# Kernel optimization log

Measured on AMD Instinct MI355X. Metric: run time of the kernel, lower is better.

The kernel has to match this reference:

```python
import jax, jax.numpy as jnp
import numpy as np

NUM_HEADS = 16
D_MODEL = 1024
HEAD_DIM = D_MODEL // NUM_HEADS
SCALE = float(np.sqrt(HEAD_DIM))  # NOTE: original multiplies q by sqrt(head_dim)
EPS = 1e-5


def layernorm(x, g, b):
    # LayerNorm over last dim (head_dim), learnable affine
    mu = jnp.mean(x, axis=-1, keepdims=True)
    var = jnp.mean(jnp.square(x - mu), axis=-1, keepdims=True)
    return (x - mu) * jax.lax.rsqrt(var + EPS) * g + b


def setup_inputs() -> dict:
    key = jax.random.key(0)
    ks = jax.random.split(key, 8)
    B, Nq, Nc = 2, 2048, 2048
    s = 0.02
    return {
        "x_query": jax.random.normal(ks[0], (B, Nq, D_MODEL), jnp.float32),
        "x_context": jax.random.normal(ks[1], (B, Nc, D_MODEL), jnp.float32),
        "Wq": jax.random.normal(ks[2], (D_MODEL, D_MODEL), jnp.float32) * s,
        "Wkv": jax.random.normal(ks[3], (D_MODEL, 2 * D_MODEL), jnp.float32) * s,
        "Wp": jax.random.normal(ks[4], (D_MODEL, D_MODEL), jnp.float32) * s,
        "bp": jnp.zeros((D_MODEL,), jnp.float32),
        "ln_g": jnp.ones((HEAD_DIM,), jnp.float32),
        "ln_b": jnp.zeros((HEAD_DIM,), jnp.float32),
    }


def reference(x_query, x_context, Wq, Wkv, Wp, bp, ln_g, ln_b):
    B, Nq, _ = x_query.shape
    Nc = x_context.shape[1]
    H, D = NUM_HEADS, HEAD_DIM
    # projections
    q = (x_query @ Wq).reshape(B, Nq, H, D).transpose(0, 2, 1, 3)  # b h n d
    kv = (x_context @ Wkv).reshape(B, Nc, 2, H, D)
    k = kv[:, :, 0].transpose(0, 2, 1, 3)  # b h n d
    v = kv[:, :, 1].transpose(0, 2, 1, 3)
    # QK-LayerNorm (shared params)
    q = layernorm(q, ln_g, ln_b)
    k = layernorm(k, ln_g, ln_b)
    # NOTE: faithful to source — q is MULTIPLIED by sqrt(head_dim)
    q = q * SCALE
    attn = jnp.einsum("bhqd,bhkd->bhqk", q, k)
    attn = jax.nn.softmax(attn, axis=-1)
    out = jnp.einsum("bhqk,bhkd->bhqd", attn, v)
    out = out.transpose(0, 2, 1, 3).reshape(B, Nq, H * D)
    return out @ Wp + bp
```

## Files before the change

kernel.cpp:

```cpp
#include <hip/hip_runtime.h>
#include <stdint.h>

#define NUM_HEADS 16
#define HEAD_DIM 64
#define D_MODEL 1024
#define SEQ 2048
#define BATCH 2

typedef unsigned short u16;
typedef __bf16 bf16x8 __attribute__((ext_vector_type(8)));
typedef _Float16 f16x8 __attribute__((ext_vector_type(8)));
typedef float f32x4 __attribute__((ext_vector_type(4)));

__device__ __forceinline__ u16 f2bf(float f) {
    union { float f; uint32_t u; } v; v.f = f;
    uint32_t u = v.u;
    u += 0x7FFFu + ((u >> 16) & 1u);
    return (u16)(u >> 16);
}
__device__ __forceinline__ float bf2f(u16 h) {
    union { uint32_t u; float f; } v; v.u = (uint32_t)h << 16; return v.f;
}
__device__ __forceinline__ u16 f2h(float f) {
    _Float16 h = (_Float16)f;
    return __builtin_bit_cast(u16, h);
}
__device__ __forceinline__ uint32_t pkrtz(float a, float b) {
    return __builtin_bit_cast(uint32_t, __builtin_amdgcn_cvt_pkrtz(a, b));
}

__device__ __forceinline__ bf16x8 ld8(const u16* p) {
    return *reinterpret_cast<const bf16x8*>(p);
}
__device__ __forceinline__ f16x8 ld8h(const u16* p) {
    return *reinterpret_cast<const f16x8*>(p);
}

__device__ __forceinline__ void gl_lds16(const void* g, void* l) {
    __builtin_amdgcn_global_load_lds(
        (const __attribute__((address_space(1))) void*)g,
        (__attribute__((address_space(3))) void*)l,
        16, 0, 0);
}

template <int CTRL>
__device__ __forceinline__ float dpp_mov(float x) {
    return __builtin_bit_cast(float,
        __builtin_amdgcn_update_dpp(0, __builtin_bit_cast(int, x), CTRL, 0xf, 0xf, true));
}
__device__ __forceinline__ float rowsum16(float x) {
    x += dpp_mov<0x121>(x);
    x += dpp_mov<0x122>(x);
    x += dpp_mov<0x124>(x);
    x += dpp_mov<0x128>(x);
    return x;
}

__global__ __launch_bounds__(256) void k_prep(const float* __restrict__ xq,
                                              const float* __restrict__ xc,
                                              const float* __restrict__ Wq,
                                              const float* __restrict__ Wkv,
                                              const float* __restrict__ Wp,
                                              u16* __restrict__ xq16,
                                              u16* __restrict__ xc16,
                                              u16* __restrict__ WqT16,
                                              u16* __restrict__ WkvT16,
                                              u16* __restrict__ WpT16) {
    __shared__ float tile[32][33];
    const int t = blockIdx.x;
    if (t < 8192) {
        int i = t * 256 + threadIdx.x;
        const float* src; u16* dst; int j;
        if (i < 1048576) { src = xq; dst = xq16; j = i; }
        else             { src = xc; dst = xc16; j = i - 1048576; }
        float4 v = reinterpret_cast<const float4*>(src)[j];
        ushort4 o;
        o.x = f2h(v.x); o.y = f2h(v.y); o.z = f2h(v.z); o.w = f2h(v.w);
        reinterpret_cast<ushort4*>(dst)[j] = o;
        return;
    }
    const float* W; u16* WT; int N, bi;
    if (t < 9216)       { W = Wq;  WT = WqT16;  N = 1024; bi = t - 8192; }
    else if (t < 11264) { W = Wkv; WT = WkvT16; N = 2048; bi = t - 9216; }
    else                { W = Wp;  WT = WpT16;  N = 1024; bi = t - 11264; }
    const int K = 1024;
    const int nb = N / 32;
    const int bn = (bi % nb) * 32, bk = (bi / nb) * 32;
    const int tx = threadIdx.x & 31;
    const int ty = threadIdx.x >> 5;
#pragma unroll
    for (int i = 0; i < 32; i += 8)
        tile[ty + i][tx] = W[(size_t)(bk + ty + i) * N + bn + tx];
    __syncthreads();
#pragma unroll
    for (int i = 0; i < 32; i += 8)
        WT[(size_t)(bn + ty + i) * K + bk + tx] = f2h(tile[tx][ty + i]);
}

__device__ __forceinline__ void gemm_mainloop_f16(const u16* __restrict__ A,
                                                  const u16* __restrict__ Bt,
                                                  u16* As, u16* Bs,
                                                  int tileM, int tileN, int K,
                                                  f32x4 acc[4][4]) {
    const int tid = threadIdx.x;
    const int lane = tid & 63;
    const int wv = tid >> 6;
    const int wm = wv >> 1, wn = wv & 1;
    const int quad = lane >> 4, l15 = lane & 15;

    const int c0 = tid, c1 = tid + 256;
    const u16* Ap0 = A + (size_t)(tileM + (c0 >> 2)) * K + (c0 & 3) * 8;
    const u16* Ap1 = A + (size_t)(tileM + (c1 >> 2)) * K + (c1 & 3) * 8;
    const u16* Bp0 = Bt + (size_t)(tileN + (c0 >> 2)) * K + (c0 & 3) * 8;
    const u16* Bp1 = Bt + (size_t)(tileN + (c1 >> 2)) * K + (c1 & 3) * 8;

    for (int k0 = 0; k0 < K; k0 += 32) {
        __syncthreads();
        gl_lds16(Ap0 + k0, &As[c0 * 8]);
        gl_lds16(Ap1 + k0, &As[c1 * 8]);
        gl_lds16(Bp0 + k0, &Bs[c0 * 8]);
        gl_lds16(Bp1 + k0, &Bs[c1 * 8]);
        __syncthreads();
        f16x8 af[4], bfr[4];
#pragma unroll
        for (int mi = 0; mi < 4; ++mi)
            af[mi] = ld8h(&As[(wm * 64 + mi * 16 + l15) * 32 + quad * 8]);
#pragma unroll
        for (int ni = 0; ni < 4; ++ni)
            bfr[ni] = ld8h(&Bs[(wn * 64 + ni * 16 + l15) * 32 + quad * 8]);
#pragma unroll
        for (int mi = 0; mi < 4; ++mi)
#pragma unroll
            for (int ni = 0; ni < 4; ++ni)
                acc[mi][ni] = __builtin_amdgcn_mfma_f32_16x16x32_f16(
                    af[mi], bfr[ni], acc[mi][ni], 0, 0, 0);
    }
}

#define ACC_INIT()                                                   \
    f32x4 acc[4][4];                                                 \
    _Pragma("unroll") for (int i = 0; i < 4; ++i)                    \
        _Pragma("unroll") for (int j = 0; j < 4; ++j)                \
            acc[i][j] = (f32x4){0.f, 0.f, 0.f, 0.f};

__global__ __launch_bounds__(256, 2) void k_proj_f16(const u16* __restrict__ xq16,
                                                     const u16* __restrict__ xc16,
                                                     const u16* __restrict__ WqT16,
                                                     const u16* __restrict__ WkvT16,
                                                     const float* __restrict__ lng,
                                                     const float* __restrict__ lnb,
                                                     u16* __restrict__ Qh_h,
                                                     u16* __restrict__ Qh_l,
                                                     u16* __restrict__ Kh_h,
                                                     u16* __restrict__ Kh_l,
                                                     u16* __restrict__ VT) {
    __shared__ __align__(16) u16 As[128 * 32];
    __shared__ __align__(16) u16 Bs[128 * 32];
    const int bx = blockIdx.x;
    const int tileM = blockIdx.y * 128;
    const int tid = threadIdx.x;
    const int lane = tid & 63;
    const int wv = tid >> 6;
    const int wm = wv >> 1, wn = wv & 1;
    const int quad = lane >> 4, l15 = lane & 15;
    ACC_INIT();

    if (bx < 16) {
        const bool isQ = bx < 8;
        const int tileN = (bx & 7) * 128;
        const u16* Axx = isQ ? xq16 : xc16;
        const u16* Bt  = isQ ? WqT16 : WkvT16;
        u16* Dh = isQ ? Qh_h : Kh_h;
        u16* Dl = isQ ? Qh_l : Kh_l;
        const float scl = isQ ? 8.0f : 1.0f;

        gemm_mainloop_f16(Axx, Bt, As, Bs, tileM, tileN, D_MODEL, acc);

        float gv[4], bv[4];
#pragma unroll
        for (int ni = 0; ni < 4; ++ni) { gv[ni] = lng[ni * 16 + l15]; bv[ni] = lnb[ni * 16 + l15]; }

#pragma unroll
        for (int mi = 0; mi < 4; ++mi) {
#pragma unroll
            for (int r = 0; r < 4; ++r) {
                float sum = 0.f, sq = 0.f;
#pragma unroll
                for (int ni = 0; ni < 4; ++ni) { float x = acc[mi][ni][r]; sum += x; sq += x * x; }
                sum = rowsum16(sum);
                sq  = rowsum16(sq);
                float mu = sum * (1.f / 64.f);
                float var = sq * (1.f / 64.f) - mu * mu;
                float rs = rsqrtf(var + 1e-5f);
                int m = tileM + wm * 64 + mi * 16 + quad * 4 + r;
                int bb = m >> 11, n = m & (SEQ - 1);
#pragma unroll
                for (int ni = 0; ni < 4; ++ni) {
                    int colg = tileN + wn * 64 + ni * 16 + l15;
                    int h = colg >> 6;
                    float y = ((acc[mi][ni][r] - mu) * rs * gv[ni] + bv[ni]) * scl;
                    size_t idx = (((size_t)bb * NUM_HEADS + h) * SEQ + n) * HEAD_DIM + (colg & 63);
                    u16 yh = f2bf(y);
                    Dh[idx] = yh;
                    Dl[idx] = f2bf(y - bf2f(yh));
                }
            }
        }
    } else {
        const int tileN = D_MODEL + (bx - 16) * 128;
        gemm_mainloop_f16(xc16, WkvT16, As, Bs, tileM, tileN, D_MODEL, acc);
#pragma unroll
        for (int mi = 0; mi < 4; ++mi) {
            int m0 = tileM + wm * 64 + mi * 16 + quad * 4;
            int bb = m0 >> 11, n0 = m0 & (SEQ - 1);
#pragma unroll
            for (int ni = 0; ni < 4; ++ni) {
                int colg = tileN + wn * 64 + ni * 16 + l15 - D_MODEL;
                int h = colg >> 6, d = colg & 63;
                ushort4 o;
                o.x = f2h(acc[mi][ni][0]);
                o.y = f2h(acc[mi][ni][1]);
                o.z = f2h(acc[mi][ni][2]);
                o.w = f2h(acc[mi][ni][3]);
                *reinterpret_cast<ushort4*>(
                    &VT[(((size_t)bb * NUM_HEADS + h) * HEAD_DIM + d) * SEQ + n0]) = o;
            }
        }
    }
}

__global__ __launch_bounds__(256, 2) void k_gemm_out(const u16* __restrict__ A,
                                                     const u16* __restrict__ Bt,
                                                     const float* __restrict__ bp,
                                                     float* __restrict__ out) {
    __shared__ __align__(16) u16 As[128 * 32];
    __shared__ __align__(16) u16 Bs[128 * 32];
    const int tileM = blockIdx.y * 128, tileN = blockIdx.x * 128;
    const int tid = threadIdx.x;
    const int lane = tid & 63;
    const int wv = tid >> 6;
    const int wm = wv >> 1, wn = wv & 1;
    const int quad = lane >> 4, l15 = lane & 15;
    ACC_INIT();
    gemm_mainloop_f16(A, Bt, As, Bs, tileM, tileN, D_MODEL, acc);

    float bpv[4];
#pragma unroll
    for (int ni = 0; ni < 4; ++ni) bpv[ni] = bp[tileN + wn * 64 + ni * 16 + l15];
#pragma unroll
    for (int mi = 0; mi < 4; ++mi) {
#pragma unroll
        for (int r = 0; r < 4; ++r) {
            int m = tileM + wm * 64 + mi * 16 + quad * 4 + r;
#pragma unroll
            for (int ni = 0; ni < 4; ++ni) {
                int colg = tileN + wn * 64 + ni * 16 + l15;
                out[(size_t)m * D_MODEL + colg] = acc[mi][ni][r] + bpv[ni];
            }
        }
    }
}

__global__ __launch_bounds__(256) void k_attn(const u16* __restrict__ Qh_h,
                                              const u16* __restrict__ Qh_l,
                                              const u16* __restrict__ Kh_h,
                                              const u16* __restrict__ Kh_l,
                                              const u16* __restrict__ VT,
                                              u16* __restrict__ AO) {
    __shared__ __align__(16) u16 Ksh[2 * 64 * 64];
    __shared__ __align__(16) u16 Ksl[2 * 64 * 64];
    __shared__ __align__(16) u16 Vs[2 * 64 * 64];
    __shared__ __align__(16) u16 Ps[64 * 72];

    const int tid = threadIdx.x;
    const int lane = tid & 63;
    const int wv = tid >> 6;
    const int quad = lane >> 4, l15 = lane & 15;
    const int id = blockIdx.x;
    const int bh = (id & 7) | (((id >> 8) & 3) << 3);
    const int qt = (id >> 3) & 31;

    const size_t bh_off = (size_t)bh * SEQ * HEAD_DIM;
    const u16* Qbh_h = Qh_h + bh_off;
    const u16* Qbh_l = Qh_l + bh_off;
    const u16* Vbh = VT + (size_t)bh * HEAD_DIM * SEQ;

    bf16x8 qfh[2], qfl[2];
#pragma unroll
    for (int kt = 0; kt < 2; ++kt) {
        size_t off = (size_t)(qt * 64 + wv * 16 + l15) * HEAD_DIM + kt * 32 + quad * 8;
        qfh[kt] = ld8(Qbh_h + off);
        qfl[kt] = ld8(Qbh_l + off);
    }

    const int rr = lane >> 3;
    const int ss = lane & 7;
    const int cc = ss ^ rr;
    const int row0 = wv * 16 + rr;
    const u16* kh0 = Kh_h + bh_off + (size_t)row0 * HEAD_DIM + cc * 8;
    const u16* kl0 = Kh_l + bh_off + (size_t)row0 * HEAD_DIM + cc * 8;
    const u16* v0  = Vbh + (size_t)row0 * SEQ + cc * 8;
    const int ldsW = (wv * 16) * 64;

    f32x4 acc_o[4];
    float m_i = -3.0e38f, l_i = 0.f;
#pragma unroll
    for (int ni = 0; ni < 4; ++ni) acc_o[ni] = (f32x4){0.f, 0.f, 0.f, 0.f};

    {
        gl_lds16(kh0,                 &Ksh[ldsW]);
        gl_lds16(kh0 + 8 * HEAD_DIM,  &Ksh[ldsW + 8 * 64]);
        gl_lds16(kl0,                 &Ksl[ldsW]);
        gl_lds16(kl0 + 8 * HEAD_DIM,  &Ksl[ldsW + 8 * 64]);
        gl_lds16(v0,                  &Vs[ldsW]);
        gl_lds16(v0 + 8 * SEQ,        &Vs[ldsW + 8 * 64]);
    }

    for (int j = 0; j < SEQ / 64; ++j) {
        __syncthreads();
        if (j + 1 < SEQ / 64) {
            const int nb = (j + 1) & 1;
            const size_t ko = (size_t)(j + 1) * 64 * HEAD_DIM;
            const int vo = (j + 1) * 64;
            gl_lds16(kh0 + ko,                 &Ksh[nb * 4096 + ldsW]);
            gl_lds16(kh0 + ko + 8 * HEAD_DIM,  &Ksh[nb * 4096 + ldsW + 8 * 64]);
            gl_lds16(kl0 + ko,                 &Ksl[nb * 4096 + ldsW]);
            gl_lds16(kl0 + ko + 8 * HEAD_DIM,  &Ksl[nb * 4096 + ldsW + 8 * 64]);
            gl_lds16(v0 + vo,                  &Vs[nb * 4096 + ldsW]);
            gl_lds16(v0 + vo + 8 * SEQ,        &Vs[nb * 4096 + ldsW + 8 * 64]);
        }
        const int bb = (j & 1) * 4096;

        f32x4 acc_s[4];
#pragma unroll
        for (int ni = 0; ni < 4; ++ni) acc_s[ni] = (f32x4){0.f, 0.f, 0.f, 0.f};
#pragma unroll
        for (int kt = 0; kt < 2; ++kt) {
            bf16x8 kfh[4], kfl[4];
#pragma unroll
            for (int ni = 0; ni < 4; ++ni) {
                int slot = (kt * 4 + quad) ^ (l15 & 7);
                kfh[ni] = ld8(&Ksh[bb + (ni * 16 + l15) * 64 + slot * 8]);
                kfl[ni] = ld8(&Ksl[bb + (ni * 16 + l15) * 64 + slot * 8]);
            }
#pragma unroll
            for (int ni = 0; ni < 4; ++ni) {
                acc_s[ni] = __builtin_amdgcn_mfma_f32_16x16x32_bf16(
                    kfh[ni], qfh[kt], acc_s[ni], 0, 0, 0);
                acc_s[ni] = __builtin_amdgcn_mfma_f32_16x16x32_bf16(
                    kfh[ni], qfl[kt], acc_s[ni], 0, 0, 0);
                acc_s[ni] = __builtin_amdgcn_mfma_f32_16x16x32_bf16(
                    kfl[ni], qfh[kt], acc_s[ni], 0, 0, 0);
            }
        }

        float mx = acc_s[0][0];
#pragma unroll
        for (int ni = 0; ni < 4; ++ni)
#pragma unroll
            for (int r = 0; r < 4; ++r) mx = fmaxf(mx, acc_s[ni][r]);
        mx = fmaxf(mx, __shfl_xor(mx, 16, 64));
        mx = fmaxf(mx, __shfl_xor(mx, 32, 64));
        float mnew = fmaxf(m_i, mx);
        float alpha = __expf(m_i - mnew);
        float sum = 0.f;
        const int psBase = (wv * 16 + l15) * 72;
#pragma unroll
        for (int ni = 0; ni < 4; ++ni) {
            float p0 = __expf(acc_s[ni][0] - mnew);
            float p1 = __expf(acc_s[ni][1] - mnew);
            float p2 = __expf(acc_s[ni][2] - mnew);
            float p3 = __expf(acc_s[ni][3] - mnew);
            sum += (p0 + p1) + (p2 + p3);
            uint2 u;
            u.x = pkrtz(p0, p1);
            u.y = pkrtz(p2, p3);
            *reinterpret_cast<uint2*>(&Ps[psBase + ni * 16 + quad * 4]) = u;
        }
        sum += __shfl_xor(sum, 16, 64);
        sum += __shfl_xor(sum, 32, 64);
        m_i = mnew;
        l_i = l_i * alpha + sum;
#pragma unroll
        for (int ni = 0; ni < 4; ++ni) acc_o[ni] *= alpha;

#pragma unroll
        for (int kt = 0; kt < 2; ++kt) {
            f16x8 pf = ld8h(&Ps[psBase + kt * 32 + quad * 8]);
            f16x8 vf[4];
#pragma unroll
            for (int ni = 0; ni < 4; ++ni) {
                int slot = (kt * 4 + quad) ^ (l15 & 7);
                vf[ni] = ld8h(&Vs[bb + (ni * 16 + l15) * 64 + slot * 8]);
            }
#pragma unroll
            for (int ni = 0; ni < 4; ++ni)
                acc_o[ni] = __builtin_amdgcn_mfma_f32_16x16x32_f16(
                    vf[ni], pf, acc_o[ni], 0, 0, 0);
        }
    }

    const float inv = 1.0f / l_i;
    const int psBase = (wv * 16 + l15) * 72;
#pragma unroll
    for (int ni = 0; ni < 4; ++ni) {
        uint2 u;
        u.x = pkrtz(acc_o[ni][0] * inv, acc_o[ni][1] * inv);
        u.y = pkrtz(acc_o[ni][2] * inv, acc_o[ni][3] * inv);
        *reinterpret_cast<uint2*>(&Ps[psBase + ni * 16 + quad * 4]) = u;
    }
    const int b = bh >> 4, h = bh & 15;
    const int qrow = qt * 64 + wv * 16 + l15;
    uint4 o0 = *reinterpret_cast<const uint4*>(&Ps[psBase + quad * 16]);
    uint4 o1 = *reinterpret_cast<const uint4*>(&Ps[psBase + quad * 16 + 8]);
    size_t outb = ((size_t)(b * SEQ + qrow)) * D_MODEL + h * 64 + quad * 16;
    *reinterpret_cast<uint4*>(&AO[outb])     = o0;
    *reinterpret_cast<uint4*>(&AO[outb + 8]) = o1;
}

extern "C" void kernel_launch(void* const* d_in, const int* in_sizes, int n_in,
                              void* d_out, int out_size, void* d_ws, size_t ws_size,
                              hipStream_t stream) {
    const float* xq  = (const float*)d_in[0];
    const float* xc  = (const float*)d_in[1];
    const float* Wq  = (const float*)d_in[2];
    const float* Wkv = (const float*)d_in[3];
    const float* Wp  = (const float*)d_in[4];
    const float* bp  = (const float*)d_in[5];
    const float* lng = (const float*)d_in[6];
    const float* lnb = (const float*)d_in[7];
    float* out = (float*)d_out;

    char* ws = (char*)d_ws;
    const size_t MB = 1 << 20;
    u16* xq16   = (u16*)(ws + 0 * MB);
    u16* xc16   = (u16*)(ws + 8 * MB);
    u16* WqT16  = (u16*)(ws + 16 * MB);
    u16* WkvT16 = (u16*)(ws + 18 * MB);
    u16* WpT16  = (u16*)(ws + 22 * MB);
    u16* Qh_h   = (u16*)(ws + 24 * MB);
    u16* Qh_l   = (u16*)(ws + 32 * MB);
    u16* Kh_h   = (u16*)(ws + 40 * MB);
    u16* Kh_l   = (u16*)(ws + 48 * MB);
    u16* VT     = (u16*)(ws + 56 * MB);
    u16* AO     = xq16;

    k_prep<<<12288, 256, 0, stream>>>(xq, xc, Wq, Wkv, Wp,
                                      xq16, xc16, WqT16, WkvT16, WpT16);
    k_proj_f16<<<dim3(24, 32), 256, 0, stream>>>(xq16, xc16, WqT16, WkvT16,
                                                 lng, lnb, Qh_h, Qh_l, Kh_h, Kh_l, VT);
    k_attn<<<1024, 256, 0, stream>>>(Qh_h, Qh_l, Kh_h, Kh_l, VT, AO);
    k_gemm_out<<<dim3(8, 32), 256, 0, stream>>>(AO, WpT16, bp, out);
}
```

Before: 274.7 us.

## Use fp16 split-Q with single fp16 K in attention, swizzle P buffer

Replaces the bf16 hi/lo split for both Q and K with fp16, keeping a hi/lo split only for Q and a single fp16 K. This cuts the QK^T MFMAs from three to two per tile, halves K global traffic and K LDS footprint, and removes the Kl staging. The P scratch buffer drops its padding and uses an XOR swizzle to avoid bank conflicts while shrinking LDS. The trade is lower precision on K, since fp16 has a narrower exponent range, which relies on the layernormed K being well-bounded.

```diff
diff --git a/kernel.cpp b/kernel.cpp
--- a/kernel.cpp
+++ b/kernel.cpp
@@ -8,30 +8,20 @@
 #define BATCH 2
 
 typedef unsigned short u16;
-typedef __bf16 bf16x8 __attribute__((ext_vector_type(8)));
 typedef _Float16 f16x8 __attribute__((ext_vector_type(8)));
 typedef float f32x4 __attribute__((ext_vector_type(4)));
 
-__device__ __forceinline__ u16 f2bf(float f) {
-    union { float f; uint32_t u; } v; v.f = f;
-    uint32_t u = v.u;
-    u += 0x7FFFu + ((u >> 16) & 1u);
-    return (u16)(u >> 16);
-}
-__device__ __forceinline__ float bf2f(u16 h) {
-    union { uint32_t u; float f; } v; v.u = (uint32_t)h << 16; return v.f;
-}
 __device__ __forceinline__ u16 f2h(float f) {
     _Float16 h = (_Float16)f;
     return __builtin_bit_cast(u16, h);
 }
+__device__ __forceinline__ float h2f(u16 h) {
+    return (float)__builtin_bit_cast(_Float16, h);
+}
 __device__ __forceinline__ uint32_t pkrtz(float a, float b) {
     return __builtin_bit_cast(uint32_t, __builtin_amdgcn_cvt_pkrtz(a, b));
 }
 
-__device__ __forceinline__ bf16x8 ld8(const u16* p) {
-    return *reinterpret_cast<const bf16x8*>(p);
-}
 __device__ __forceinline__ f16x8 ld8h(const u16* p) {
     return *reinterpret_cast<const f16x8*>(p);
 }
@@ -151,8 +141,7 @@
                                                      const float* __restrict__ lnb,
                                                      u16* __restrict__ Qh_h,
                                                      u16* __restrict__ Qh_l,
-                                                     u16* __restrict__ Kh_h,
-                                                     u16* __restrict__ Kh_l,
+                                                     u16* __restrict__ Kh,
                                                      u16* __restrict__ VT) {
     __shared__ __align__(16) u16 As[128 * 32];
     __shared__ __align__(16) u16 Bs[128 * 32];
@@ -170,8 +159,6 @@
         const int tileN = (bx & 7) * 128;
         const u16* Axx = isQ ? xq16 : xc16;
         const u16* Bt  = isQ ? WqT16 : WkvT16;
-        u16* Dh = isQ ? Qh_h : Kh_h;
-        u16* Dl = isQ ? Qh_l : Kh_l;
         const float scl = isQ ? 8.0f : 1.0f;
 
         gemm_mainloop_f16(Axx, Bt, As, Bs, tileM, tileN, D_MODEL, acc);
@@ -200,9 +187,13 @@
                     int h = colg >> 6;
                     float y = ((acc[mi][ni][r] - mu) * rs * gv[ni] + bv[ni]) * scl;
                     size_t idx = (((size_t)bb * NUM_HEADS + h) * SEQ + n) * HEAD_DIM + (colg & 63);
-                    u16 yh = f2bf(y);
-                    Dh[idx] = yh;
-                    Dl[idx] = f2bf(y - bf2f(yh));
+                    u16 yh = f2h(y);
+                    if (isQ) {
+                        Qh_h[idx] = yh;
+                        Qh_l[idx] = f2h(y - h2f(yh));
+                    } else {
+                        Kh[idx] = yh;
+                    }
                 }
             }
         }
@@ -263,43 +254,39 @@
 
 __global__ __launch_bounds__(256) void k_attn(const u16* __restrict__ Qh_h,
                                               const u16* __restrict__ Qh_l,
-                                              const u16* __restrict__ Kh_h,
-                                              const u16* __restrict__ Kh_l,
+                                              const u16* __restrict__ Kh,
                                               const u16* __restrict__ VT,
                                               u16* __restrict__ AO) {
-    __shared__ __align__(16) u16 Ksh[2 * 64 * 64];
-    __shared__ __align__(16) u16 Ksl[2 * 64 * 64];
+    __shared__ __align__(16) u16 Ks[2 * 64 * 64];
     __shared__ __align__(16) u16 Vs[2 * 64 * 64];
-    __shared__ __align__(16) u16 Ps[64 * 72];
+    __shared__ __align__(16) u16 Ps[64 * 64];
 
     const int tid = threadIdx.x;
     const int lane = tid & 63;
     const int wv = tid >> 6;
     const int quad = lane >> 4, l15 = lane & 15;
+    const int sw = l15 & 3;
     const int id = blockIdx.x;
     const int bh = (id & 7) | (((id >> 8) & 3) << 3);
     const int qt = (id >> 3) & 31;
 
     const size_t bh_off = (size_t)bh * SEQ * HEAD_DIM;
-    const u16* Qbh_h = Qh_h + bh_off;
-    const u16* Qbh_l = Qh_l + bh_off;
     const u16* Vbh = VT + (size_t)bh * HEAD_DIM * SEQ;
 
-    bf16x8 qfh[2], qfl[2];
+    f16x8 qfh[2], qfl[2];
 #pragma unroll
     for (int kt = 0; kt < 2; ++kt) {
-        size_t off = (size_t)(qt * 64 + wv * 16 + l15) * HEAD_DIM + kt * 32 + quad * 8;
-        qfh[kt] = ld8(Qbh_h + off);
-        qfl[kt] = ld8(Qbh_l + off);
+        size_t off = bh_off + (size_t)(qt * 64 + wv * 16 + l15) * HEAD_DIM + kt * 32 + quad * 8;
+        qfh[kt] = ld8h(Qh_h + off);
+        qfl[kt] = ld8h(Qh_l + off);
     }
 
     const int rr = lane >> 3;
     const int ss = lane & 7;
     const int cc = ss ^ rr;
     const int row0 = wv * 16 + rr;
-    const u16* kh0 = Kh_h + bh_off + (size_t)row0 * HEAD_DIM + cc * 8;
-    const u16* kl0 = Kh_l + bh_off + (size_t)row0 * HEAD_DIM + cc * 8;
-    const u16* v0  = Vbh + (size_t)row0 * SEQ + cc * 8;
+    const u16* k0 = Kh + bh_off + (size_t)row0 * HEAD_DIM + cc * 8;
+    const u16* v0 = Vbh + (size_t)row0 * SEQ + cc * 8;
     const int ldsW = (wv * 16) * 64;
 
     f32x4 acc_o[4];
@@ -307,14 +294,12 @@
 #pragma unroll
     for (int ni = 0; ni < 4; ++ni) acc_o[ni] = (f32x4){0.f, 0.f, 0.f, 0.f};
 
-    {
-        gl_lds16(kh0,                 &Ksh[ldsW]);
-        gl_lds16(kh0 + 8 * HEAD_DIM,  &Ksh[ldsW + 8 * 64]);
-        gl_lds16(kl0,                 &Ksl[ldsW]);
-        gl_lds16(kl0 + 8 * HEAD_DIM,  &Ksl[ldsW + 8 * 64]);
-        gl_lds16(v0,                  &Vs[ldsW]);
-        gl_lds16(v0 + 8 * SEQ,        &Vs[ldsW + 8 * 64]);
-    }
+    gl_lds16(k0,                &Ks[ldsW]);
+    gl_lds16(k0 + 8 * HEAD_DIM, &Ks[ldsW + 8 * 64]);
+    gl_lds16(v0,                &Vs[ldsW]);
+    gl_lds16(v0 + 8 * SEQ,      &Vs[ldsW + 8 * 64]);
+
+    const int psRow = (wv * 16 + l15) * 64;
 
     for (int j = 0; j < SEQ / 64; ++j) {
         __syncthreads();
@@ -322,12 +307,10 @@
             const int nb = (j + 1) & 1;
             const size_t ko = (size_t)(j + 1) * 64 * HEAD_DIM;
             const int vo = (j + 1) * 64;
-            gl_lds16(kh0 + ko,                 &Ksh[nb * 4096 + ldsW]);
-            gl_lds16(kh0 + ko + 8 * HEAD_DIM,  &Ksh[nb * 4096 + ldsW + 8 * 64]);
-            gl_lds16(kl0 + ko,                 &Ksl[nb * 4096 + ldsW]);
-            gl_lds16(kl0 + ko + 8 * HEAD_DIM,  &Ksl[nb * 4096 + ldsW + 8 * 64]);
-            gl_lds16(v0 + vo,                  &Vs[nb * 4096 + ldsW]);
-            gl_lds16(v0 + vo + 8 * SEQ,        &Vs[nb * 4096 + ldsW + 8 * 64]);
+            gl_lds16(k0 + ko,                &Ks[nb * 4096 + ldsW]);
+            gl_lds16(k0 + ko + 8 * HEAD_DIM, &Ks[nb * 4096 + ldsW + 8 * 64]);
+            gl_lds16(v0 + vo,                &Vs[nb * 4096 + ldsW]);
+            gl_lds16(v0 + vo + 8 * SEQ,      &Vs[nb * 4096 + ldsW + 8 * 64]);
         }
         const int bb = (j & 1) * 4096;
 
@@ -336,21 +319,18 @@
         for (int ni = 0; ni < 4; ++ni) acc_s[ni] = (f32x4){0.f, 0.f, 0.f, 0.f};
 #pragma unroll
         for (int kt = 0; kt < 2; ++kt) {
-            bf16x8 kfh[4], kfl[4];
+            f16x8 kf[4];
 #pragma unroll
             for (int ni = 0; ni < 4; ++ni) {
                 int slot = (kt * 4 + quad) ^ (l15 & 7);
-                kfh[ni] = ld8(&Ksh[bb + (ni * 16 + l15) * 64 + slot * 8]);
-                kfl[ni] = ld8(&Ksl[bb + (ni * 16 + l15) * 64 + slot * 8]);
+                kf[ni] = ld8h(&Ks[bb + (ni * 16 + l15) * 64 + slot * 8]);
             }
 #pragma unroll
             for (int ni = 0; ni < 4; ++ni) {
-                acc_s[ni] = __builtin_amdgcn_mfma_f32_16x16x32_bf16(
-                    kfh[ni], qfh[kt], acc_s[ni], 0, 0, 0);
-                acc_s[ni] = __builtin_amdgcn_mfma_f32_16x16x32_bf16(
-                    kfh[ni], qfl[kt], acc_s[ni], 0, 0, 0);
-                acc_s[ni] = __builtin_amdgcn_mfma_f32_16x16x32_bf16(
-                    kfl[ni], qfh[kt], acc_s[ni], 0, 0, 0);
+                acc_s[ni] = __builtin_amdgcn_mfma_f32_16x16x32_f16(
+                    kf[ni], qfh[kt], acc_s[ni], 0, 0, 0);
+                acc_s[ni] = __builtin_amdgcn_mfma_f32_16x16x32_f16(
+                    kf[ni], qfl[kt], acc_s[ni], 0, 0, 0);
             }
         }
 
@@ -364,7 +344,6 @@
         float mnew = fmaxf(m_i, mx);
         float alpha = __expf(m_i - mnew);
         float sum = 0.f;
-        const int psBase = (wv * 16 + l15) * 72;
 #pragma unroll
         for (int ni = 0; ni < 4; ++ni) {
             float p0 = __expf(acc_s[ni][0] - mnew);
@@ -375,7 +354,7 @@
             uint2 u;
             u.x = pkrtz(p0, p1);
             u.y = pkrtz(p2, p3);
-            *reinterpret_cast<uint2*>(&Ps[psBase + ni * 16 + quad * 4]) = u;
+            *reinterpret_cast<uint2*>(&Ps[psRow + ((ni ^ sw) * 16) + quad * 4]) = u;
         }
         sum += __shfl_xor(sum, 16, 64);
         sum += __shfl_xor(sum, 32, 64);
@@ -386,7 +365,8 @@
 
 #pragma unroll
         for (int kt = 0; kt < 2; ++kt) {
-            f16x8 pf = ld8h(&Ps[psBase + kt * 32 + quad * 8]);
+            int pchunk = (kt * 2 + (quad >> 1)) ^ sw;
+            f16x8 pf = ld8h(&Ps[psRow + pchunk * 16 + (quad & 1) * 8]);
             f16x8 vf[4];
 #pragma unroll
             for (int ni = 0; ni < 4; ++ni) {
@@ -401,18 +381,18 @@
     }
 
     const float inv = 1.0f / l_i;
-    const int psBase = (wv * 16 + l15) * 72;
 #pragma unroll
     for (int ni = 0; ni < 4; ++ni) {
         uint2 u;
         u.x = pkrtz(acc_o[ni][0] * inv, acc_o[ni][1] * inv);
         u.y = pkrtz(acc_o[ni][2] * inv, acc_o[ni][3] * inv);
-        *reinterpret_cast<uint2*>(&Ps[psBase + ni * 16 + quad * 4]) = u;
+        *reinterpret_cast<uint2*>(&Ps[psRow + ((ni ^ sw) * 16) + quad * 4]) = u;
     }
     const int b = bh >> 4, h = bh & 15;
     const int qrow = qt * 64 + wv * 16 + l15;
-    uint4 o0 = *reinterpret_cast<const uint4*>(&Ps[psBase + quad * 16]);
-    uint4 o1 = *reinterpret_cast<const uint4*>(&Ps[psBase + quad * 16 + 8]);
+    const int echunk = quad ^ sw;
+    uint4 o0 = *reinterpret_cast<const uint4*>(&Ps[psRow + echunk * 16]);
+    uint4 o1 = *reinterpret_cast<const uint4*>(&Ps[psRow + echunk * 16 + 8]);
     size_t outb = ((size_t)(b * SEQ + qrow)) * D_MODEL + h * 64 + quad * 16;
     *reinterpret_cast<uint4*>(&AO[outb])     = o0;
     *reinterpret_cast<uint4*>(&AO[outb + 8]) = o1;
@@ -440,15 +420,14 @@
     u16* WpT16  = (u16*)(ws + 22 * MB);
     u16* Qh_h   = (u16*)(ws + 24 * MB);
     u16* Qh_l   = (u16*)(ws + 32 * MB);
-    u16* Kh_h   = (u16*)(ws + 40 * MB);
-    u16* Kh_l   = (u16*)(ws + 48 * MB);
-    u16* VT     = (u16*)(ws + 56 * MB);
+    u16* Kh     = (u16*)(ws + 40 * MB);
+    u16* VT     = (u16*)(ws + 48 * MB);
     u16* AO     = xq16;
 
     k_prep<<<12288, 256, 0, stream>>>(xq, xc, Wq, Wkv, Wp,
                                       xq16, xc16, WqT16, WkvT16, WpT16);
     k_proj_f16<<<dim3(24, 32), 256, 0, stream>>>(xq16, xc16, WqT16, WkvT16,
-                                                 lng, lnb, Qh_h, Qh_l, Kh_h, Kh_l, VT);
-    k_attn<<<1024, 256, 0, stream>>>(Qh_h, Qh_l, Kh_h, Kh_l, VT, AO);
+                                                 lng, lnb, Qh_h, Qh_l, Kh, VT);
+    k_attn<<<1024, 256, 0, stream>>>(Qh_h, Qh_l, Kh, VT, AO);
     k_gemm_out<<<dim3(8, 32), 256, 0, stream>>>(AO, WpT16, bp, out);
 }
```

After: 262.2 us. 1.05x faster.
